# Optimization experiments

Measured on AMD Instinct MI355X. Metric: run time of the kernel, lower is better.

Reference implementation:

```python
import jax, jax.numpy as jnp
import numpy as np

D, DFF, H, K = 512, 2048, 8, 31
DK = D // H
EPS = 1e-5


def _ln(x, g, b):
    m = jnp.mean(x, axis=-1, keepdims=True)
    v = jnp.mean((x - m) ** 2, axis=-1, keepdims=True)
    return (x - m) * jax.lax.rsqrt(v + EPS) * g + b


def _ffn(x, w1, b1, w2, b2):
    return jax.nn.silu(x @ w1 + b1) @ w2 + b2


def _rel_shift(x):
    # x: (B, H, T, P) with P = 2T-1
    b, h, q, p = x.shape
    x = jnp.pad(x, ((0, 0), (0, 0), (0, 0), (1, 0)))
    x = x.reshape(b, h, p + 1, q)[:, :, 1:, :]
    return x.reshape(b, h, q, p)


def setup_inputs() -> dict:
    key = jax.random.key(0)
    ks = jax.random.split(key, 32)
    r = lambda i, shape: 0.02 * jax.random.normal(ks[i], shape, dtype=jnp.float32)
    B, T = 4, 1024
    inp = {
        'x': jax.random.normal(ks[0], (B, T, D), dtype=jnp.float32),
        'pos_emb': jax.random.normal(ks[1], (1, 2 * T - 1, D), dtype=jnp.float32),
        # LayerNorms (5)
        'ln1_g': jnp.ones((D,)), 'ln1_b': jnp.zeros((D,)),
        'ln2_g': jnp.ones((D,)), 'ln2_b': jnp.zeros((D,)),
        'ln3_g': jnp.ones((D,)), 'ln3_b': jnp.zeros((D,)),
        'ln4_g': jnp.ones((D,)), 'ln4_b': jnp.zeros((D,)),
        'ln5_g': jnp.ones((D,)), 'ln5_b': jnp.zeros((D,)),
        # FFN1
        'ff1_w1': r(2, (D, DFF)), 'ff1_b1': jnp.zeros((DFF,)),
        'ff1_w2': r(3, (DFF, D)), 'ff1_b2': jnp.zeros((D,)),
        # Attention
        'wq': r(4, (D, D)), 'bq': jnp.zeros((D,)),
        'wk': r(5, (D, D)), 'bk': jnp.zeros((D,)),
        'wv': r(6, (D, D)), 'bv': jnp.zeros((D,)),
        'wp': r(7, (D, D)),
        'wo': r(8, (D, D)), 'bo': jnp.zeros((D,)),
        'pos_u': r(9, (H, DK)), 'pos_v': r(10, (H, DK)),
        # Conv module
        'pw1_w': r(11, (2 * D, D)), 'pw1_b': jnp.zeros((2 * D,)),
        'dw_w': r(12, (D, 1, K)), 'dw_b': jnp.zeros((D,)),
        'bn_g': jnp.ones((D,)), 'bn_b': jnp.zeros((D,)),
        'pw2_w': r(13, (D, D)), 'pw2_b': jnp.zeros((D,)),
        # FFN2
        'ff2_w1': r(14, (D, DFF)), 'ff2_b1': jnp.zeros((DFF,)),
        'ff2_w2': r(15, (DFF, D)), 'ff2_b2': jnp.zeros((D,)),
    }
    return inp


def _attn(x, pos_emb, wq, bq, wk, bk, wv, bv, wp, wo, bo, pos_u, pos_v):
    B, T, _ = x.shape
    q = (x @ wq + bq).reshape(B, T, H, DK).transpose(0, 2, 1, 3)
    k = (x @ wk + bk).reshape(B, T, H, DK).transpose(0, 2, 1, 3)
    v = (x @ wv + bv).reshape(B, T, H, DK).transpose(0, 2, 1, 3)
    P = pos_emb.shape[1]
    p = (pos_emb[0] @ wp).reshape(P, H, DK)  # (P, H, DK)
    ac = jnp.einsum('bhqd,bhkd->bhqk', q + pos_u[:, None, :], k)
    bd = jnp.einsum('bhqd,phd->bhqp', q + pos_v[:, None, :], p)
    bd = _rel_shift(bd)[:, :, :, :T]
    scores = (ac + bd) * (DK ** -0.5)
    attn = jax.nn.softmax(scores, axis=-1)
    out = jnp.einsum('bhqk,bhkd->bhqd', attn, v)
    out = out.transpose(0, 2, 1, 3).reshape(B, T, D)
    return out @ wo + bo


def _conv(x, pw1_w, pw1_b, dw_w, dw_b, bn_g, bn_b, pw2_w, pw2_b):
    y = x.transpose(0, 2, 1)  # (B, D, T)
    y = jnp.einsum('od,bdt->bot', pw1_w, y) + pw1_b[:, None]
    a, g = jnp.split(y, 2, axis=1)
    y = a * jax.nn.sigmoid(g)  # GLU
    pad = (K - 1) // 2
    y = jax.lax.conv_general_dilated(
        y, dw_w, (1,), [(pad, pad)],
        dimension_numbers=('NCW', 'OIW', 'NCW'), feature_group_count=D)
    y = y + dw_b[:, None]
    m = jnp.mean(y, axis=(0, 2), keepdims=True)
    var = jnp.mean((y - m) ** 2, axis=(0, 2), keepdims=True)
    y = (y - m) * jax.lax.rsqrt(var + EPS) * bn_g[:, None] + bn_b[:, None]
    y = jax.nn.silu(y)
    y = jnp.einsum('od,bdt->bot', pw2_w, y) + pw2_b[:, None]
    return y.transpose(0, 2, 1)


def reference(x, pos_emb,
              ln1_g, ln1_b, ff1_w1, ff1_b1, ff1_w2, ff1_b2,
              ln2_g, ln2_b, wq, bq, wk, bk, wv, bv, wp, wo, bo, pos_u, pos_v,
              ln3_g, ln3_b, pw1_w, pw1_b, dw_w, dw_b, bn_g, bn_b, pw2_w, pw2_b,
              ln4_g, ln4_b, ff2_w1, ff2_b1, ff2_w2, ff2_b2,
              ln5_g, ln5_b):
    h = x + 0.5 * _ffn(_ln(x, ln1_g, ln1_b), ff1_w1, ff1_b1, ff1_w2, ff1_b2)
    h = h + _attn(_ln(h, ln2_g, ln2_b), pos_emb, wq, bq, wk, bk, wv, bv, wp, wo, bo, pos_u, pos_v)
    h = h + _conv(_ln(h, ln3_g, ln3_b), pw1_w, pw1_b, dw_w, dw_b, bn_g, bn_b, pw2_w, pw2_b)
    h = h + 0.5 * _ffn(_ln(h, ln4_g, ln4_b), ff2_w1, ff2_b1, ff2_w2, ff2_b2)
    return _ln(h, ln5_g, ln5_b)
```

## Files before the change

### kernel.cpp

```cpp
#include <hip/hip_runtime.h>
#include <math.h>

#define TT   1024
#define BBZ  4
#define DD   512
#define DFF_ 2048
#define HH   8
#define DKK  64
#define NTOK 4096
#define EPSF 1e-5f
#define MB   1048576
#define QSCALE 0.18033688011112042f
#define M0OFF  24.0f

typedef unsigned short u16;
typedef __attribute__((ext_vector_type(8))) short s8v;
typedef __attribute__((ext_vector_type(4))) float f32x4;
typedef __attribute__((ext_vector_type(4))) unsigned short us4;
typedef __attribute__((ext_vector_type(8))) unsigned short us8;

__device__ __forceinline__ float b2f(u16 v){
    union { unsigned int u; float f; } x; x.u = ((unsigned int)v) << 16; return x.f;
}
__device__ __forceinline__ u16 f2b(float f){
    union { float f; unsigned int u; } x; x.f = f;
    unsigned int r = x.u + 0x7fffu + ((x.u >> 16) & 1u);
    return (u16)(r >> 16);
}
__device__ __forceinline__ float sigmoidf_(float x){ return 1.0f/(1.0f+__expf(-x)); }

__device__ __forceinline__ void gld16(const u16* g, u16* l){
    __builtin_amdgcn_global_load_lds(
        (const __attribute__((address_space(1))) unsigned int*)g,
        (__attribute__((address_space(3))) unsigned int*)l, 16, 0, 0);
}

template<int OMODE>
__global__ __launch_bounds__(256) void bgemm128(
    const u16* __restrict__ A, int lda,
    const u16* __restrict__ B, int ldb,
    void* __restrict__ Cv, int ldc, int K,
    const float* __restrict__ bias, int act,
    const float* __restrict__ posu, const float* __restrict__ posv)
{
    int n0 = blockIdx.x * 128;
    int m0 = blockIdx.y * 128;

    __shared__ u16 As[128*64];
    __shared__ u16 Bs[128*64];

    int t = threadIdx.x;
    int w = t >> 6, l = t & 63;
    int lrow = l >> 3, lslot = l & 7;
    int kswz = (lslot ^ lrow) * 8;
    int wm = w >> 1, wn = w & 1;
    int lr = l & 15, lk = l >> 4;

    f32x4 acc[4][4] = {};

    for (int k0 = 0; k0 < K; k0 += 64){
        #pragma unroll
        for (int it = 0; it < 4; ++it){
            int rb = it*32 + w*8;
            gld16(A + (size_t)(m0 + rb + lrow)*lda + k0 + kswz, &As[rb*64]);
            gld16(B + (size_t)(n0 + rb + lrow)*ldb + k0 + kswz, &Bs[rb*64]);
        }
        __syncthreads();

        s8v af[2][4], bf[2][4];
        #pragma unroll
        for (int kh = 0; kh < 2; ++kh){
            int sl = (kh*4 + lk) ^ (lr & 7);
            #pragma unroll
            for (int mi = 0; mi < 4; ++mi)
                af[kh][mi] = *(const s8v*)&As[(wm*64 + mi*16 + lr)*64 + sl*8];
            #pragma unroll
            for (int ni = 0; ni < 4; ++ni)
                bf[kh][ni] = *(const s8v*)&Bs[(wn*64 + ni*16 + lr)*64 + sl*8];
        }
        #pragma unroll
        for (int kh = 0; kh < 2; ++kh)
            #pragma unroll
            for (int mi = 0; mi < 4; ++mi)
                #pragma unroll
                for (int ni = 0; ni < 4; ++ni)
                    acc[mi][ni] = __builtin_amdgcn_mfma_f32_16x16x32_bf16(
                        af[kh][mi], bf[kh][ni], acc[mi][ni], 0, 0, 0);
        __syncthreads();
    }

    #pragma unroll
    for (int mi = 0; mi < 4; ++mi){
        #pragma unroll
        for (int ni = 0; ni < 4; ++ni){
            int gn = n0 + wn*64 + ni*16 + lr;
            float bval = bias ? bias[gn] : 0.0f;
            #pragma unroll
            for (int r = 0; r < 4; ++r){
                int gm = m0 + wm*64 + mi*16 + lk*4 + r;
                float vv = acc[mi][ni][r] + bval;
                if (act) vv = vv * sigmoidf_(vv);
                if (OMODE == 1){
                    ((u16*)Cv)[(size_t)gm*ldc + gn] = f2b(vv);
                } else if (OMODE == 5){
                    u16* base = (u16*)Cv;
                    if (gn < 512){
                        size_t idx = (size_t)gm*512 + gn;
                        base[idx]              = f2b((vv + posu[gn])*QSCALE);
                        base[idx + (2u<<20)]   = f2b((vv + posv[gn])*QSCALE);
                    } else if (gn < 1024){
                        base[(4u<<20) + (size_t)gm*512 + (gn-512)] = f2b(vv);
                    } else {
                        int gnp = gn - 1024;
                        int bb = gm >> 10, tt2 = gm & 1023;
                        size_t idx = (((size_t)(bb*8 + (gnp>>6)))*64 + (gnp&63))*1024 + tt2;
                        base[(6u<<20) + idx] = f2b(vv);
                    }
                } else {
                    u16* base = (u16*)Cv;
                    size_t idx = (gn < 512)
                        ? ((size_t)gm*512 + gn)*2
                        : ((size_t)gm*512 + (gn-512))*2 + 1;
                    base[idx] = f2b(vv);
                }
            }
        }
    }
}

template<int OMODE>
__global__ __launch_bounds__(256) void bgemm64(
    const u16* __restrict__ A, int lda,
    const u16* __restrict__ B, int ldb,
    u16* __restrict__ C, int ldc, int K,
    const float* __restrict__ bias, float alpha,
    const u16* __restrict__ resid)
{
    int n0 = blockIdx.x * 64;
    int m0 = blockIdx.y * 64;

    __shared__ u16 As[64*64];
    __shared__ u16 Bs[64*64];

    int t = threadIdx.x;
    int w = t >> 6, l = t & 63;
    int lrow = l >> 3, lslot = l & 7;
    int kswz = (lslot ^ lrow) * 8;
    int wm = w >> 1, wn = w & 1;
    int lr = l & 15, lk = l >> 4;

    f32x4 acc[2][2] = {};

    for (int k0 = 0; k0 < K; k0 += 64){
        #pragma unroll
        for (int it = 0; it < 2; ++it){
            int rb = it*32 + w*8;
            gld16(A + (size_t)(m0 + rb + lrow)*lda + k0 + kswz, &As[rb*64]);
            gld16(B + (size_t)(n0 + rb + lrow)*ldb + k0 + kswz, &Bs[rb*64]);
        }
        __syncthreads();

        s8v af[2][2], bf[2][2];
        #pragma unroll
        for (int kh = 0; kh < 2; ++kh){
            int sl = (kh*4 + lk) ^ (lr & 7);
            #pragma unroll
            for (int mi = 0; mi < 2; ++mi)
                af[kh][mi] = *(const s8v*)&As[(wm*32 + mi*16 + lr)*64 + sl*8];
            #pragma unroll
            for (int ni = 0; ni < 2; ++ni)
                bf[kh][ni] = *(const s8v*)&Bs[(wn*32 + ni*16 + lr)*64 + sl*8];
        }
        #pragma unroll
        for (int kh = 0; kh < 2; ++kh)
            #pragma unroll
            for (int mi = 0; mi < 2; ++mi)
                #pragma unroll
                for (int ni = 0; ni < 2; ++ni)
                    acc[mi][ni] = __builtin_amdgcn_mfma_f32_16x16x32_bf16(
                        af[kh][mi], bf[kh][ni], acc[mi][ni], 0, 0, 0);
        __syncthreads();
    }

    #pragma unroll
    for (int mi = 0; mi < 2; ++mi){
        #pragma unroll
        for (int ni = 0; ni < 2; ++ni){
            int gn = n0 + wn*32 + ni*16 + lr;
            float bval = bias ? bias[gn] : 0.0f;
            #pragma unroll
            for (int r = 0; r < 4; ++r){
                int gm = m0 + wm*32 + mi*16 + lk*4 + r;
                float vv = acc[mi][ni][r] + bval;
                if (OMODE == 0){
                    vv *= alpha;
                    if (resid) vv += b2f(resid[(size_t)gm*ldc + gn]);
                }
                C[(size_t)gm*ldc + gn] = f2b(vv);
            }
        }
    }
}

__global__ __launch_bounds__(256) void bgemm64k(
    const u16* __restrict__ A, int lda,
    const u16* __restrict__ B, int ldb,
    u16* __restrict__ C, int ldc, int K,
    const float* __restrict__ bias, float alpha,
    const float* __restrict__ residF, const u16* __restrict__ residB)
{
    int n0 = blockIdx.x * 64;
    int m0 = blockIdx.y * 64;

    __shared__ u16 As[64*128];
    __shared__ u16 Bs[64*128];

    int t = threadIdx.x;
    int w = t >> 6, l = t & 63;
    int r4 = l >> 4;
    int s16 = l & 15;
    int kswz = (s16 ^ (w*4 + r4)) * 8;
    int wm = w >> 1, wn = w & 1;
    int lr = l & 15, lk = l >> 4;

    f32x4 acc[2][2] = {};

    for (int k0 = 0; k0 < K; k0 += 128){
        #pragma unroll
        for (int cb = 0; cb < 4; ++cb){
            int rowu = cb*16 + w*4;
            gld16(A + (size_t)(m0 + rowu + r4)*lda + k0 + kswz, &As[rowu*128]);
            gld16(B + (size_t)(n0 + rowu + r4)*ldb + k0 + kswz, &Bs[rowu*128]);
        }
        __syncthreads();

        #pragma unroll
        for (int kh = 0; kh < 4; ++kh){
            int sl = ((kh*4 + lk) ^ lr) * 8;
            s8v af[2], bf[2];
            #pragma unroll
            for (int mi = 0; mi < 2; ++mi)
                af[mi] = *(const s8v*)&As[(wm*32 + mi*16 + lr)*128 + sl];
            #pragma unroll
            for (int ni = 0; ni < 2; ++ni)
                bf[ni] = *(const s8v*)&Bs[(wn*32 + ni*16 + lr)*128 + sl];
            #pragma unroll
            for (int mi = 0; mi < 2; ++mi)
                #pragma unroll
                for (int ni = 0; ni < 2; ++ni)
                    acc[mi][ni] = __builtin_amdgcn_mfma_f32_16x16x32_bf16(
                        af[mi], bf[ni], acc[mi][ni], 0, 0, 0);
        }
        __syncthreads();
    }

    #pragma unroll
    for (int mi = 0; mi < 2; ++mi){
        #pragma unroll
        for (int ni = 0; ni < 2; ++ni){
            int gn = n0 + wn*32 + ni*16 + lr;
            float bval = bias ? bias[gn] : 0.0f;
            #pragma unroll
            for (int r = 0; r < 4; ++r){
                int gm = m0 + wm*32 + mi*16 + lk*4 + r;
                float vv = (acc[mi][ni][r] + bval) * alpha;
                size_t idx = (size_t)gm*ldc + gn;
                if (residF) vv += residF[idx];
                if (residB) vv += b2f(residB[idx]);
                C[idx] = f2b(vv);
            }
        }
    }
}

__global__ __launch_bounds__(256) void attn_fused(
    const u16* __restrict__ qub, const u16* __restrict__ qvb,
    const u16* __restrict__ kb,  const u16* __restrict__ vt,
    const u16* __restrict__ pp,  u16* __restrict__ out)
{
    int z = blockIdx.y;
    int b = z >> 3, hh = z & 7;
    int i0 = blockIdx.x * 64;

    __shared__ u16 Kb2[2][64*64];
    __shared__ u16 Vb2[2][64*64];
    __shared__ u16 Pring[3][64*64];
    __shared__ u16 PT[64*64];
    __shared__ float Bandd[4][1024];

    int t = threadIdx.x;
    int w = t >> 6, l = t & 63;
    int lrow = l >> 3, lslot = l & 7;
    int kswz = (lslot ^ lrow) * 8;
    int lr = l & 15, lk = l >> 4;

    #pragma unroll
    for (int it = 0; it < 2; ++it){
        int rb = it*32 + w*8;
        gld16(qub + (size_t)(b*TT + i0 + rb + lrow)*DD + hh*64 + kswz, &PT[rb*64]);
        gld16(qvb + (size_t)(b*TT + i0 + rb + lrow)*DD + hh*64 + kswz,
              (u16*)&Bandd[0][0] + rb*64);
    }
    __syncthreads();
    s8v af_u[2], af_v[2];
    #pragma unroll
    for (int kh = 0; kh < 2; ++kh){
        int sl = (kh*4 + lk) ^ (lr & 7);
        af_u[kh] = *(const s8v*)&PT[(w*16 + lr)*64 + sl*8];
        af_v[kh] = *(const s8v*)((const u16*)&Bandd[0][0] + (w*16 + lr)*64 + sl*8);
    }
    #pragma unroll
    for (int it = 0; it < 2; ++it){
        int rb = it*32 + w*8;
        gld16(kb + (size_t)(b*TT +        rb + lrow)*DD + hh*64 + kswz, &Kb2[0][rb*64]);
        gld16(vt + ((size_t)z*64 + rb + lrow)*TT +                kswz, &Vb2[0][rb*64]);
        gld16(pp + (size_t)(960  - i0 +   rb + lrow)*DD + hh*64 + kswz, &Pring[0][rb*64]);
        gld16(pp + (size_t)(1024 - i0 +   rb + lrow)*DD + hh*64 + kswz, &Pring[1][rb*64]);
    }

    f32x4 o_[4] = {};
    float Lp[4] = {0.f, 0.f, 0.f, 0.f};

    int s0 = 0, s1 = 1, s2 = 2;

    for (int jt = 0; jt < 16; ++jt){
        int cur = jt & 1;
        __syncthreads();

        if (jt < 15){
            #pragma unroll
            for (int it = 0; it < 2; ++it){
                int rb = it*32 + w*8;
                gld16(kb + (size_t)(b*TT + (jt+1)*64 + rb + lrow)*DD + hh*64 + kswz,
                      &Kb2[cur^1][rb*64]);
                gld16(vt + ((size_t)z*64 + rb + lrow)*TT + (jt+1)*64 + kswz,
                      &Vb2[cur^1][rb*64]);
                gld16(pp + (size_t)(960 + (jt+2)*64 - i0 + rb + lrow)*DD + hh*64 + kswz,
                      &Pring[s2][rb*64]);
            }
        }

        f32x4 sac[4] = {};
        f32x4 g[5] = {};
        __builtin_amdgcn_s_setprio(1);
        #pragma unroll
        for (int kh = 0; kh < 2; ++kh){
            int sl = (kh*4 + lk) ^ (lr & 7);
            #pragma unroll
            for (int n = 0; n < 4; ++n){
                s8v bK = *(const s8v*)&Kb2[cur][(n*16 + lr)*64 + sl*8];
                sac[n] = __builtin_amdgcn_mfma_f32_16x16x32_bf16(af_u[kh], bK, sac[n], 0,0,0);
            }
            #pragma unroll
            for (int n = 0; n < 5; ++n){
                int nn = (3 - w) + n;
                const u16* pc = (nn & 4) ? &Pring[s1][0] : &Pring[s0][0];
                s8v bP = *(const s8v*)&pc[(((nn&3)*16) + lr)*64 + sl*8];
                g[n] = __builtin_amdgcn_mfma_f32_16x16x32_bf16(af_v[kh], bP, g[n], 0,0,0);
            }
        }
        __builtin_amdgcn_s_setprio(0);

        {
            int c0 = (3 - w)*16 + lr;
            int d  = (c0 - 63) & 63;
            int sb = (lk*4 + ((d >> 1) & 3)*4) & 15;
            f32x4 vv;
            #pragma unroll
            for (int r = 0; r < 4; ++r){
                int iia = w*16 + lk*4 + r;
                vv[r] = (iia >= 63 - c0) ? g[0][r] : g[4][r];
            }
            *(f32x4*)&Bandd[w][d*16 + sb] = vv;
        }
        #pragma unroll
        for (int n = 1; n < 4; ++n){
            int c = (3 - w + n)*16 + lr;
            int d = (c - 63) & 63;
            int sb = (lk*4 + ((d >> 1) & 3)*4) & 15;
            *(f32x4*)&Bandd[w][d*16 + sb] = g[n];
        }

        float p_[4][4];
        #pragma unroll
        for (int r = 0; r < 4; ++r){
            int ii_l = lk*4 + r;
            float rs = 0.0f;
            #pragma unroll
            for (int n = 0; n < 4; ++n){
                int jj = n*16 + lr;
                int d  = (jj - 16*w - ii_l) & 63;
                float bd = Bandd[w][d*16 + ((ii_l + ((d>>1)&3)*4) & 15)];
                float pv = __builtin_amdgcn_exp2f(sac[n][r] + bd - M0OFF);
                p_[n][r] = pv; rs += pv;
            }
            Lp[r] += rs;
        }

        #pragma unroll
        for (int n = 0; n < 4; ++n)
            #pragma unroll
            for (int r = 0; r < 4; ++r){
                int ii  = w*16 + lk*4 + r;
                int col = n*16 + lr;
                int sl  = (col>>3) ^ (ii&7);
                PT[ii*64 + sl*8 + (col&7)] = f2b(p_[n][r]);
            }

        __builtin_amdgcn_s_setprio(1);
        #pragma unroll
        for (int kh = 0; kh < 2; ++kh){
            int sl = (kh*4 + lk) ^ (lr & 7);
            s8v ap = *(const s8v*)&PT[(w*16 + lr)*64 + sl*8];
            #pragma unroll
            for (int n = 0; n < 4; ++n){
                s8v bV = *(const s8v*)&Vb2[cur][(n*16 + lr)*64 + sl*8];
                o_[n] = __builtin_amdgcn_mfma_f32_16x16x32_bf16(ap, bV, o_[n], 0,0,0);
            }
        }
        __builtin_amdgcn_s_setprio(0);
        int tmp = s0; s0 = s1; s1 = s2; s2 = tmp;
    }

    float Lr[4];
    #pragma unroll
    for (int r = 0; r < 4; ++r){
        float Lv = Lp[r];
        #pragma unroll
        for (int msk = 1; msk < 16; msk <<= 1) Lv += __shfl_xor(Lv, msk);
        Lr[r] = 1.0f / Lv;
    }

    #pragma unroll
    for (int n = 0; n < 4; ++n)
        #pragma unroll
        for (int r = 0; r < 4; ++r){
            int i  = i0 + w*16 + lk*4 + r;
            int dk = n*16 + lr;
            out[(size_t)(b*TT + i)*DD + hh*64 + dk] = f2b(o_[n][r] * Lr[r]);
        }
}

template<int IB, int OB>
__global__ __launch_bounds__(256) void ln_kernel(const void* __restrict__ inp,
    const float* __restrict__ g, const float* __restrict__ b, void* __restrict__ outv)
{
    int w = threadIdx.x >> 6, l = threadIdx.x & 63;
    int row = blockIdx.x*4 + w;
    float v[8];
    if (IB){
        us8 xv = ((const us8*)((const u16*)inp + (size_t)row*DD))[l];
        #pragma unroll
        for (int e=0;e<8;e++) v[e] = b2f(xv[e]);
    } else {
        const float4* xr = (const float4*)((const float*)inp + (size_t)row*DD);
        float4 a = xr[2*l], c = xr[2*l+1];
        v[0]=a.x; v[1]=a.y; v[2]=a.z; v[3]=a.w;
        v[4]=c.x; v[5]=c.y; v[6]=c.z; v[7]=c.w;
    }
    float s = 0.f, q = 0.f;
    #pragma unroll
    for (int e=0;e<8;e++){ s += v[e]; q += v[e]*v[e]; }
    #pragma unroll
    for (int msk = 1; msk < 64; msk <<= 1){
        s += __shfl_xor(s, msk);
        q += __shfl_xor(q, msk);
    }
    float mean = s*(1.0f/DD);
    float var  = q*(1.0f/DD) - mean*mean;
    float rinv = rsqrtf(var+EPSF);
    float4 g0 = ((const float4*)g)[2*l], g1 = ((const float4*)g)[2*l+1];
    float4 b0 = ((const float4*)b)[2*l], b1 = ((const float4*)b)[2*l+1];
    float gv[8] = {g0.x,g0.y,g0.z,g0.w,g1.x,g1.y,g1.z,g1.w};
    float bv[8] = {b0.x,b0.y,b0.z,b0.w,b1.x,b1.y,b1.z,b1.w};
    float y[8];
    #pragma unroll
    for (int e=0;e<8;e++) y[e] = (v[e]-mean)*rinv*gv[e] + bv[e];
    if (OB){
        us8 o;
        #pragma unroll
        for (int e=0;e<8;e++) o[e] = f2b(y[e]);
        ((us8*)((u16*)outv + (size_t)row*DD))[l] = o;
    } else {
        float4 o0 = {y[0],y[1],y[2],y[3]};
        float4 o1 = {y[4],y[5],y[6],y[7]};
        float4* op = (float4*)((float*)outv + (size_t)row*DD);
        op[2*l] = o0; op[2*l+1] = o1;
    }
}

struct Prep9 {
    const float* s[9];
    u16* d[9];
    int R[9], C[9];
    int t0[10];
};

__global__ __launch_bounds__(256) void prep_all(Prep9 P,
    const float* __restrict__ pw1_w, const float* __restrict__ pw2_w,
    const float* __restrict__ pos_emb, const float* __restrict__ dw_w,
    const float* __restrict__ bq, const float* __restrict__ bk,
    const float* __restrict__ bv,
    u16* __restrict__ pw1b, u16* __restrict__ pw2b,
    u16* __restrict__ posb, float* __restrict__ wt, float* __restrict__ bqkv)
{
    __shared__ float tile[32][33];
    int bid = blockIdx.x;
    if (bid < 5376){
        int j = 0;
        #pragma unroll
        for (int e=1; e<9; e++) if (bid >= P.t0[e]) j = e;
        int lb = bid - P.t0[j];
        int nx = P.C[j] >> 5;
        int c0 = (lb % nx) << 5;
        int r0 = (lb / nx) << 5;
        const float* in = P.s[j];
        u16* out = P.d[j];
        int R = P.R[j], C = P.C[j];
        int tx = threadIdx.x & 31, ty = threadIdx.x >> 5;
        #pragma unroll
        for (int i=0;i<4;i++){
            int rr = ty + i*8;
            tile[rr][tx] = in[(size_t)(r0+rr)*C + c0+tx];
        }
        __syncthreads();
        #pragma unroll
        for (int i=0;i<4;i++){
            int cc = ty + i*8;
            out[(size_t)(c0+cc)*R + r0+tx] = f2b(tile[tx][cc]);
        }
        return;
    }
    int i = (bid - 5376)*256 + threadIdx.x;
    if (i < 524288) { pw1b[i] = f2b(pw1_w[i]); return; }
    i -= 524288;
    if (i < 262144) { pw2b[i] = f2b(pw2_w[i]); return; }
    i -= 262144;
    if (i < 1048576) { posb[i] = (i < 2047*512) ? f2b(pos_emb[i]) : (u16)0; return; }
    i -= 1048576;
    if (i < 15872) { int kk = i >> 9, d = i & 511; wt[i] = dw_w[d*31+kk]; return; }
    i -= 15872;
    if (i < 1536) bqkv[i] = (i < 512) ? bq[i] : (i < 1024 ? bk[i-512] : bv[i-1024]);
}

__global__ __launch_bounds__(256) void dwconv_kernel(const unsigned int* __restrict__ t2i,
    const float* __restrict__ wt, const float* __restrict__ bias, u16* __restrict__ z)
{
    int d  = blockIdx.x*256 + threadIdx.x;
    int c  = blockIdx.y;
    int b  = c >> 7;
    int t0 = (c & 127) << 3;
    const unsigned int* pa = t2i + (size_t)b*TT*512 + d;
    float wv[31];
    #pragma unroll
    for (int kk=0;kk<31;kk++) wv[kk] = wt[kk*512 + d];
    float xv[38];
    #pragma unroll
    for (int e=0;e<38;e++){
        int tp = t0 - 15 + e;
        if (tp >= 0 && tp < TT){
            unsigned int pv = pa[(size_t)tp*512];
            float a  = b2f((u16)(pv & 0xffffu));
            float gg = b2f((u16)(pv >> 16));
            xv[e] = a * sigmoidf_(gg);
        } else xv[e] = 0.0f;
    }
    float bsv = bias[d];
    #pragma unroll
    for (int j=0;j<8;j++){
        float sum = bsv;
        #pragma unroll
        for (int kk=0;kk<31;kk++) sum = fmaf(xv[j+kk], wv[kk], sum);
        z[(size_t)(b*TT+t0+j)*DD + d] = f2b(sum);
    }
}

__global__ __launch_bounds__(256) void bn_reduce2(const u16* __restrict__ z,
    float* __restrict__ stats)
{
    int bi = blockIdx.x;
    int t  = threadIdx.x;
    float s0=0.f,q0=0.f,s1=0.f,q1=0.f;
    #pragma unroll
    for (int r=0;r<16;r++){
        size_t row = (size_t)(bi*16 + r)*DD;
        float v0 = b2f(z[row + t]);
        float v1 = b2f(z[row + t + 256]);
        s0 += v0; q0 += v0*v0;
        s1 += v1; q1 += v1*v1;
    }
    atomicAdd(&stats[t],        s0);
    atomicAdd(&stats[512 + t],  q0);
    atomicAdd(&stats[t + 256],      s1);
    atomicAdd(&stats[512 + t + 256], q1);
}

__global__ __launch_bounds__(256) void bn_apply_kernel(const u16* __restrict__ z,
    const float* __restrict__ stats, const float* __restrict__ g, const float* __restrict__ b,
    u16* __restrict__ out)
{
    int idx = blockIdx.x*256 + threadIdx.x;
    int c = idx & (DD-1);
    float m   = stats[c]*(1.0f/NTOK);
    float var = stats[DD+c]*(1.0f/NTOK) - m*m;
    float vv  = (b2f(z[idx])-m)*rsqrtf(var+EPSF)*g[c] + b[c];
    out[idx]  = f2b(vv*sigmoidf_(vv));
}

extern "C" void kernel_launch(void* const* d_in, const int* in_sizes, int n_in,
                              void* d_out, int out_size, void* d_ws, size_t ws_size,
                              hipStream_t stream)
{
    const float* x       = (const float*)d_in[0];
    const float* pos_emb = (const float*)d_in[1];
    const float* ln1_g=(const float*)d_in[2],  *ln1_b=(const float*)d_in[3];
    const float* ln2_g=(const float*)d_in[4],  *ln2_b=(const float*)d_in[5];
    const float* ln3_g=(const float*)d_in[6],  *ln3_b=(const float*)d_in[7];
    const float* ln4_g=(const float*)d_in[8],  *ln4_b=(const float*)d_in[9];
    const float* ln5_g=(const float*)d_in[10], *ln5_b=(const float*)d_in[11];
    const float* ff1_w1=(const float*)d_in[12], *ff1_b1=(const float*)d_in[13];
    const float* ff1_w2=(const float*)d_in[14], *ff1_b2=(const float*)d_in[15];
    const float* wq=(const float*)d_in[16], *bq=(const float*)d_in[17];
    const float* wk=(const float*)d_in[18], *bk=(const float*)d_in[19];
    const float* wv=(const float*)d_in[20], *bv=(const float*)d_in[21];
    const float* wp=(const float*)d_in[22];
    const float* wo=(const float*)d_in[23], *bo=(const float*)d_in[24];
    const float* pos_u=(const float*)d_in[25], *pos_v=(const float*)d_in[26];
    const float* pw1_w=(const float*)d_in[27], *pw1_b=(const float*)d_in[28];
    const float* dw_w=(const float*)d_in[29],  *dw_b=(const float*)d_in[30];
    const float* bn_g=(const float*)d_in[31],  *bn_b=(const float*)d_in[32];
    const float* pw2_w=(const float*)d_in[33], *pw2_b=(const float*)d_in[34];
    const float* ff2_w1=(const float*)d_in[35], *ff2_b1=(const float*)d_in[36];
    const float* ff2_w2=(const float*)d_in[37], *ff2_b2=(const float*)d_in[38];

    char* W = (char*)d_ws;
    u16*  h     = (u16*) (W);
    u16*  xn    = (u16*) (W + (size_t) 8*MB);
    u16*  wall  = (u16*) (W + (size_t)12*MB);
    u16*  qub   = (u16*) (W + (size_t)28*MB);
    u16*  qvb   = (u16*) (W + (size_t)32*MB);
    u16*  kb    = (u16*) (W + (size_t)36*MB);
    u16*  vt    = (u16*) (W + (size_t)40*MB);
    u16*  pproj = (u16*) (W + (size_t)44*MB);
    char* big   = W + (size_t)48*MB;
    u16*  ffh   = (u16*)big;
    unsigned int* t2i = (unsigned int*)big;
    u16*  t3u   = (u16*)(big + (size_t)8*MB);
    float* stats= (float*)(W + (size_t)112*MB);
    float* wt   = stats + 4096;
    float* bqkv = wt + 15872;

    u16* ff1w1T = wall;
    u16* ff1w2T = wall + 1048576;
    u16* wqT    = wall + 2097152;
    u16* wkT    = wall + 2359296;
    u16* wvT    = wall + 2621440;
    u16* wpT    = wall + 2883584;
    u16* woT    = wall + 3145728;
    u16* ff2w1T = wall + 3407872;
    u16* ff2w2T = wall + 4456448;
    u16* pw1b   = wall + 5505024;
    u16* pw2b   = wall + 6029312;
    u16* posb   = wall + 6291456;

    dim3 blk(256);

    Prep9 P;
    P.s[0]=ff1_w1; P.d[0]=ff1w1T; P.R[0]=512;  P.C[0]=2048;
    P.s[1]=ff1_w2; P.d[1]=ff1w2T; P.R[1]=2048; P.C[1]=512;
    P.s[2]=wq;     P.d[2]=wqT;    P.R[2]=512;  P.C[2]=512;
    P.s[3]=wk;     P.d[3]=wkT;    P.R[3]=512;  P.C[3]=512;
    P.s[4]=wv;     P.d[4]=wvT;    P.R[4]=512;  P.C[4]=512;
    P.s[5]=wp;     P.d[5]=wpT;    P.R[5]=512;  P.C[5]=512;
    P.s[6]=wo;     P.d[6]=woT;    P.R[6]=512;  P.C[6]=512;
    P.s[7]=ff2_w1; P.d[7]=ff2w1T; P.R[7]=512;  P.C[7]=2048;
    P.s[8]=ff2_w2; P.d[8]=ff2w2T; P.R[8]=2048; P.C[8]=512;
    int tc[9] = {1024,1024,256,256,256,256,256,1024,1024};
    P.t0[0]=0; for (int e=0;e<9;e++) P.t0[e+1]=P.t0[e]+tc[e];
    prep_all<<<dim3(5376+7236), blk, 0, stream>>>(P, pw1_w, pw2_w, pos_emb, dw_w,
                                                  bq, bk, bv,
                                                  pw1b, pw2b, posb, wt, bqkv);

    ln_kernel<0,1><<<dim3(NTOK/4), blk, 0, stream>>>(x, ln1_g, ln1_b, xn);
    bgemm128<1><<<dim3(16,32), blk, 0, stream>>>(xn,512, ff1w1T,512,
        ffh,2048, 512, ff1_b1,1, nullptr,nullptr);
    bgemm64k<<<dim3(8,64), blk, 0, stream>>>(ffh,2048, ff1w2T,2048,
        h,512, 2048, ff1_b2,0.5f, x, nullptr);

    ln_kernel<1,1><<<dim3(NTOK/4), blk, 0, stream>>>(h, ln2_g, ln2_b, xn);
    bgemm128<5><<<dim3(12,32), blk, 0, stream>>>(xn,512, wqT,512,
        qub,512, 512, bqkv,0, pos_u,pos_v);
    bgemm64<1><<<dim3(8,32), blk, 0, stream>>>(posb,512, wpT,512,
        pproj,512, 512, nullptr,1.f, nullptr);

    attn_fused<<<dim3(16,32), blk, 0, stream>>>(qub, qvb, kb, vt, pproj, xn);

    bgemm64<0><<<dim3(8,64), blk, 0, stream>>>(xn,512, woT,512,
        h,512, 512, bo,1.f, h);

    ln_kernel<1,1><<<dim3(NTOK/4), blk, 0, stream>>>(h, ln3_g, ln3_b, xn);
    bgemm128<6><<<dim3(8,32), blk, 0, stream>>>(xn,512, pw1b,512,
        t2i,1024, 512, pw1_b,0, nullptr,nullptr);
    dwconv_kernel<<<dim3(2,512), blk, 0, stream>>>(t2i, wt, dw_b, t3u);
    (void)hipMemsetAsync(stats, 0, 4096, stream);
    bn_reduce2<<<dim3(256), blk, 0, stream>>>(t3u, stats);
    bn_apply_kernel<<<dim3(NTOK*DD/256), blk, 0, stream>>>(t3u, stats, bn_g, bn_b, xn);
    bgemm64<0><<<dim3(8,64), blk, 0, stream>>>(xn,512, pw2b,512,
        h,512, 512, pw2_b,1.f, h);

    ln_kernel<1,1><<<dim3(NTOK/4), blk, 0, stream>>>(h, ln4_g, ln4_b, xn);
    bgemm128<1><<<dim3(16,32), blk, 0, stream>>>(xn,512, ff2w1T,512,
        ffh,2048, 512, ff2_b1,1, nullptr,nullptr);
    bgemm64k<<<dim3(8,64), blk, 0, stream>>>(ffh,2048, ff2w2T,2048,
        h,512, 2048, ff2_b2,0.5f, nullptr, h);

    ln_kernel<1,0><<<dim3(NTOK/4), blk, 0, stream>>>(h, ln5_g, ln5_b, (float*)d_out);
}
```

Before: 276.7 us.

## Fuse QKV and positional GEMMs, fold BN stats into dwconv, reswizzle band LDS

Merges the QKV projection and the positional-embedding projection into one launch by assigning extra block columns to the pos GEMM. It also accumulates the BatchNorm sum and sum-of-squares inside the depthwise conv kernel through atomics, which removes the separate bn_reduce pass over the conv output. Finally it changes the swizzle of the Bandd LDS buffer in attention, permuting the stored float4 lanes so the later scalar reads hit fewer bank conflicts. In exchange there are more atomics (per-thread, per-channel), some idle blocks in the fused GEMM grid, and extra select logic in the attention store.

```diff
diff --git a/kernel.cpp b/kernel.cpp
--- a/kernel.cpp
+++ b/kernel.cpp
@@ -40,8 +40,7 @@
     const u16* __restrict__ A, int lda,
     const u16* __restrict__ B, int ldb,
     void* __restrict__ Cv, int ldc, int K,
-    const float* __restrict__ bias, int act,
-    const float* __restrict__ posu, const float* __restrict__ posv)
+    const float* __restrict__ bias, int act)
 {
     int n0 = blockIdx.x * 128;
     int m0 = blockIdx.y * 128;
@@ -102,8 +101,89 @@
                 if (act) vv = vv * sigmoidf_(vv);
                 if (OMODE == 1){
                     ((u16*)Cv)[(size_t)gm*ldc + gn] = f2b(vv);
-                } else if (OMODE == 5){
+                } else {
                     u16* base = (u16*)Cv;
+                    size_t idx = (gn < 512)
+                        ? ((size_t)gm*512 + gn)*2
+                        : ((size_t)gm*512 + (gn-512))*2 + 1;
+                    base[idx] = f2b(vv);
+                }
+            }
+        }
+    }
+}
+
+__global__ __launch_bounds__(256) void qkvp_gemm(
+    const u16* __restrict__ xn, const u16* __restrict__ wqT,
+    const u16* __restrict__ posb, const u16* __restrict__ wpT,
+    u16* __restrict__ qkvbase, u16* __restrict__ pproj,
+    const float* __restrict__ bqkv,
+    const float* __restrict__ posu, const float* __restrict__ posv)
+{
+    bool isP = (blockIdx.x >= 12);
+    if (isP && blockIdx.y >= 16) return;
+    const u16* A = isP ? posb : xn;
+    const u16* B = isP ? wpT : wqT;
+    int n0 = isP ? (blockIdx.x - 12)*128 : blockIdx.x*128;
+    int m0 = blockIdx.y * 128;
+
+    __shared__ u16 As[128*64];
+    __shared__ u16 Bs[128*64];
+
+    int t = threadIdx.x;
+    int w = t >> 6, l = t & 63;
+    int lrow = l >> 3, lslot = l & 7;
+    int kswz = (lslot ^ lrow) * 8;
+    int wm = w >> 1, wn = w & 1;
+    int lr = l & 15, lk = l >> 4;
+
+    f32x4 acc[4][4] = {};
+
+    for (int k0 = 0; k0 < 512; k0 += 64){
+        #pragma unroll
+        for (int it = 0; it < 4; ++it){
+            int rb = it*32 + w*8;
+            gld16(A + (size_t)(m0 + rb + lrow)*512 + k0 + kswz, &As[rb*64]);
+            gld16(B + (size_t)(n0 + rb + lrow)*512 + k0 + kswz, &Bs[rb*64]);
+        }
+        __syncthreads();
+
+        s8v af[2][4], bf[2][4];
+        #pragma unroll
+        for (int kh = 0; kh < 2; ++kh){
+            int sl = (kh*4 + lk) ^ (lr & 7);
+            #pragma unroll
+            for (int mi = 0; mi < 4; ++mi)
+                af[kh][mi] = *(const s8v*)&As[(wm*64 + mi*16 + lr)*64 + sl*8];
+            #pragma unroll
+            for (int ni = 0; ni < 4; ++ni)
+                bf[kh][ni] = *(const s8v*)&Bs[(wn*64 + ni*16 + lr)*64 + sl*8];
+        }
+        #pragma unroll
+        for (int kh = 0; kh < 2; ++kh)
+            #pragma unroll
+            for (int mi = 0; mi < 4; ++mi)
+                #pragma unroll
+                for (int ni = 0; ni < 4; ++ni)
+                    acc[mi][ni] = __builtin_amdgcn_mfma_f32_16x16x32_bf16(
+                        af[kh][mi], bf[kh][ni], acc[mi][ni], 0, 0, 0);
+        __syncthreads();
+    }
+
+    #pragma unroll
+    for (int mi = 0; mi < 4; ++mi){
+        #pragma unroll
+        for (int ni = 0; ni < 4; ++ni){
+            int gn = n0 + wn*64 + ni*16 + lr;
+            float bval = isP ? 0.0f : bqkv[gn];
+            #pragma unroll
+            for (int r = 0; r < 4; ++r){
+                int gm = m0 + wm*64 + mi*16 + lk*4 + r;
+                float vv = acc[mi][ni][r] + bval;
+                if (isP){
+                    pproj[(size_t)gm*512 + gn] = f2b(vv);
+                } else {
+                    u16* base = qkvbase;
                     if (gn < 512){
                         size_t idx = (size_t)gm*512 + gn;
                         base[idx]              = f2b((vv + posu[gn])*QSCALE);
@@ -116,19 +196,12 @@
                         size_t idx = (((size_t)(bb*8 + (gnp>>6)))*64 + (gnp&63))*1024 + tt2;
                         base[(6u<<20) + idx] = f2b(vv);
                     }
-                } else {
-                    u16* base = (u16*)Cv;
-                    size_t idx = (gn < 512)
-                        ? ((size_t)gm*512 + gn)*2
-                        : ((size_t)gm*512 + (gn-512))*2 + 1;
-                    base[idx] = f2b(vv);
                 }
             }
         }
     }
 }
 
-template<int OMODE>
 __global__ __launch_bounds__(256) void bgemm64(
     const u16* __restrict__ A, int lda,
     const u16* __restrict__ B, int ldb,
@@ -191,11 +264,8 @@
             #pragma unroll
             for (int r = 0; r < 4; ++r){
                 int gm = m0 + wm*32 + mi*16 + lk*4 + r;
-                float vv = acc[mi][ni][r] + bval;
-                if (OMODE == 0){
-                    vv *= alpha;
-                    if (resid) vv += b2f(resid[(size_t)gm*ldc + gn]);
-                }
+                float vv = (acc[mi][ni][r] + bval) * alpha;
+                if (resid) vv += b2f(resid[(size_t)gm*ldc + gn]);
                 C[(size_t)gm*ldc + gn] = f2b(vv);
             }
         }
@@ -361,24 +431,32 @@
         }
         __builtin_amdgcn_s_setprio(0);
 
-        {
-            int c0 = (3 - w)*16 + lr;
-            int d  = (c0 - 63) & 63;
-            int sb = (lk*4 + ((d >> 1) & 3)*4) & 15;
-            f32x4 vv;
-            #pragma unroll
-            for (int r = 0; r < 4; ++r){
-                int iia = w*16 + lk*4 + r;
-                vv[r] = (iia >= 63 - c0) ? g[0][r] : g[4][r];
-            }
-            *(f32x4*)&Bandd[w][d*16 + sb] = vv;
-        }
-        #pragma unroll
-        for (int n = 1; n < 4; ++n){
+        #pragma unroll
+        for (int n = 0; n < 4; ++n){
             int c = (3 - w + n)*16 + lr;
             int d = (c - 63) & 63;
-            int sb = (lk*4 + ((d >> 1) & 3)*4) & 15;
-            *(f32x4*)&Bandd[w][d*16 + sb] = g[n];
+            int rho = (d >> 2) & 3;
+            f32x4 vv;
+            if (n == 0){
+                #pragma unroll
+                for (int r = 0; r < 4; ++r){
+                    int iia = w*16 + lk*4 + r;
+                    vv[r] = (iia >= 63 - c) ? g[0][r] : g[4][r];
+                }
+            } else {
+                vv = g[n];
+            }
+            bool sw1 = rho & 1, sw2 = rho & 2;
+            float b0 = sw1 ? vv[1] : vv[0];
+            float b1 = sw1 ? vv[0] : vv[1];
+            float b2 = sw1 ? vv[3] : vv[2];
+            float b3 = sw1 ? vv[2] : vv[3];
+            f32x4 vvp;
+            vvp[0] = sw2 ? b2 : b0;
+            vvp[1] = sw2 ? b3 : b1;
+            vvp[2] = sw2 ? b0 : b2;
+            vvp[3] = sw2 ? b1 : b3;
+            *(f32x4*)&Bandd[w][d*16 + ((lk + d) & 3)*4] = vvp;
         }
 
         float p_[4][4];
@@ -390,7 +468,8 @@
             for (int n = 0; n < 4; ++n){
                 int jj = n*16 + lr;
                 int d  = (jj - 16*w - ii_l) & 63;
-                float bd = Bandd[w][d*16 + ((ii_l + ((d>>1)&3)*4) & 15)];
+                float bd = Bandd[w][d*16 + (((ii_l>>2) + d) & 3)*4
+                                         + ((ii_l ^ (d>>2)) & 3)];
                 float pv = __builtin_amdgcn_exp2f(sac[n][r] + bd - M0OFF);
                 p_[n][r] = pv; rs += pv;
             }
@@ -544,7 +623,8 @@
 }
 
 __global__ __launch_bounds__(256) void dwconv_kernel(const unsigned int* __restrict__ t2i,
-    const float* __restrict__ wt, const float* __restrict__ bias, u16* __restrict__ z)
+    const float* __restrict__ wt, const float* __restrict__ bias, u16* __restrict__ z,
+    float* __restrict__ stats)
 {
     int d  = blockIdx.x*256 + threadIdx.x;
     int c  = blockIdx.y;
@@ -566,33 +646,17 @@
         } else xv[e] = 0.0f;
     }
     float bsv = bias[d];
+    float s = 0.f, q = 0.f;
     #pragma unroll
     for (int j=0;j<8;j++){
         float sum = bsv;
         #pragma unroll
         for (int kk=0;kk<31;kk++) sum = fmaf(xv[j+kk], wv[kk], sum);
         z[(size_t)(b*TT+t0+j)*DD + d] = f2b(sum);
-    }
-}
-
-__global__ __launch_bounds__(256) void bn_reduce2(const u16* __restrict__ z,
-    float* __restrict__ stats)
-{
-    int bi = blockIdx.x;
-    int t  = threadIdx.x;
-    float s0=0.f,q0=0.f,s1=0.f,q1=0.f;
-    #pragma unroll
-    for (int r=0;r<16;r++){
-        size_t row = (size_t)(bi*16 + r)*DD;
-        float v0 = b2f(z[row + t]);
-        float v1 = b2f(z[row + t + 256]);
-        s0 += v0; q0 += v0*v0;
-        s1 += v1; q1 += v1*v1;
-    }
-    atomicAdd(&stats[t],        s0);
-    atomicAdd(&stats[512 + t],  q0);
-    atomicAdd(&stats[t + 256],      s1);
-    atomicAdd(&stats[512 + t + 256], q1);
+        s += sum; q += sum*sum;
+    }
+    atomicAdd(&stats[d],       s);
+    atomicAdd(&stats[512 + d], q);
 }
 
 __global__ __launch_bounds__(256) void bn_apply_kernel(const u16* __restrict__ z,
@@ -683,34 +747,31 @@
 
     ln_kernel<0,1><<<dim3(NTOK/4), blk, 0, stream>>>(x, ln1_g, ln1_b, xn);
     bgemm128<1><<<dim3(16,32), blk, 0, stream>>>(xn,512, ff1w1T,512,
-        ffh,2048, 512, ff1_b1,1, nullptr,nullptr);
+        ffh,2048, 512, ff1_b1,1);
     bgemm64k<<<dim3(8,64), blk, 0, stream>>>(ffh,2048, ff1w2T,2048,
         h,512, 2048, ff1_b2,0.5f, x, nullptr);
 
     ln_kernel<1,1><<<dim3(NTOK/4), blk, 0, stream>>>(h, ln2_g, ln2_b, xn);
-    bgemm128<5><<<dim3(12,32), blk, 0, stream>>>(xn,512, wqT,512,
-        qub,512, 512, bqkv,0, pos_u,pos_v);
-    bgemm64<1><<<dim3(8,32), blk, 0, stream>>>(posb,512, wpT,512,
-        pproj,512, 512, nullptr,1.f, nullptr);
+    qkvp_gemm<<<dim3(16,32), blk, 0, stream>>>(xn, wqT, posb, wpT,
+        qub, pproj, bqkv, pos_u, pos_v);
 
     attn_fused<<<dim3(16,32), blk, 0, stream>>>(qub, qvb, kb, vt, pproj, xn);
 
-    bgemm64<0><<<dim3(8,64), blk, 0, stream>>>(xn,512, woT,512,
+    bgemm64<<<dim3(8,64), blk, 0, stream>>>(xn,512, woT,512,
         h,512, 512, bo,1.f, h);
 
     ln_kernel<1,1><<<dim3(NTOK/4), blk, 0, stream>>>(h, ln3_g, ln3_b, xn);
     bgemm128<6><<<dim3(8,32), blk, 0, stream>>>(xn,512, pw1b,512,
-        t2i,1024, 512, pw1_b,0, nullptr,nullptr);
-    dwconv_kernel<<<dim3(2,512), blk, 0, stream>>>(t2i, wt, dw_b, t3u);
+        t2i,1024, 512, pw1_b,0);
     (void)hipMemsetAsync(stats, 0, 4096, stream);
-    bn_reduce2<<<dim3(256), blk, 0, stream>>>(t3u, stats);
+    dwconv_kernel<<<dim3(2,512), blk, 0, stream>>>(t2i, wt, dw_b, t3u, stats);
     bn_apply_kernel<<<dim3(NTOK*DD/256), blk, 0, stream>>>(t3u, stats, bn_g, bn_b, xn);
-    bgemm64<0><<<dim3(8,64), blk, 0, stream>>>(xn,512, pw2b,512,
+    bgemm64<<<dim3(8,64), blk, 0, stream>>>(xn,512, pw2b,512,
         h,512, 512, pw2_b,1.f, h);
 
     ln_kernel<1,1><<<dim3(NTOK/4), blk, 0, stream>>>(h, ln4_g, ln4_b, xn);
     bgemm128<1><<<dim3(16,32), blk, 0, stream>>>(xn,512, ff2w1T,512,
-        ffh,2048, 512, ff2_b1,1, nullptr,nullptr);
+        ffh,2048, 512, ff2_b1,1);
     bgemm64k<<<dim3(8,64), blk, 0, stream>>>(ffh,2048, ff2w2T,2048,
         h,512, 2048, ff2_b2,0.5f, nullptr, h);
 
```

Measured after the change: 265.5 us. 4.0% less time.
